# Kernel tuning notes

Hardware: AMD Instinct MI355X
Metric: run time of the kernel (lower is better)

Reference implementation:

```python
import jax, jax.numpy as jnp
import numpy as np

N_NODES = 50000
N_EDGES = 800000
IN_CH = 128
OUT_CH = 64
HID_CH = 2 * OUT_CH  # 128


def gcn_conv(x, edge_index, W, b, n_nodes):
    """PyG GCNConv: linear -> add self-loops -> sym-normalized scatter-add -> bias."""
    h = x @ W  # [N, out]
    loop = jnp.arange(n_nodes)
    row = jnp.concatenate([edge_index[0], loop])  # source nodes
    col = jnp.concatenate([edge_index[1], loop])  # target nodes
    deg = jax.ops.segment_sum(jnp.ones_like(col, dtype=h.dtype), col, num_segments=n_nodes)
    dinv = jnp.where(deg > 0, jax.lax.rsqrt(jnp.maximum(deg, 1.0)), 0.0)
    norm = dinv[row] * dinv[col]  # [E+N]
    msg = h[row] * norm[:, None]  # gather + scale, [E+N, out]
    out = jax.ops.segment_sum(msg, col, num_segments=n_nodes)  # scatter-add
    return out + b


def setup_inputs() -> dict:
    key = jax.random.key(0)
    ks = jax.random.split(key, 9)
    x = jax.random.normal(ks[0], (N_NODES, IN_CH), dtype=jnp.float32)
    edge_index = jax.random.randint(ks[1], (2, N_EDGES), 0, N_NODES, dtype=jnp.int64)
    s_in = 1.0 / np.sqrt(IN_CH)
    s_hid = 1.0 / np.sqrt(HID_CH)
    W1 = jax.random.normal(ks[2], (IN_CH, HID_CH), dtype=jnp.float32) * s_in
    b1 = jnp.zeros((HID_CH,), dtype=jnp.float32)
    W2 = jax.random.normal(ks[3], (HID_CH, OUT_CH), dtype=jnp.float32) * s_hid
    b2 = jnp.zeros((OUT_CH,), dtype=jnp.float32)
    W3 = jax.random.normal(ks[4], (HID_CH, OUT_CH), dtype=jnp.float32) * s_hid
    b3 = jnp.zeros((OUT_CH,), dtype=jnp.float32)
    return {"x": x, "edge_index": edge_index, "W1": W1, "b1": b1,
            "W2": W2, "b2": b2, "W3": W3, "b3": b3}


def reference(x, edge_index, W1, b1, W2, b2, W3, b3):
    act = jax.nn.relu
    hidden = act(gcn_conv(x, edge_index, W1, b1, N_NODES))
    x1 = act(gcn_conv(hidden, edge_index, W2, b2, N_NODES))
    x2 = act(gcn_conv(hidden, edge_index, W3, b3, N_NODES))
    return (x1, x2)
```

## Files before the change

kernel.cpp:

```cpp
#include <hip/hip_runtime.h>

#define N_NODES 50000
#define N_EDGES 800000
#define CH 128
#define SCAN_BLKS 98
#define WT_PAD 136
#define DUMMY N_NODES

typedef __attribute__((ext_vector_type(8))) short short8;
typedef __attribute__((ext_vector_type(4))) float floatx4;

__device__ __forceinline__ short f2bf(float f) {
    union { float f; unsigned u; } v; v.f = f;
    unsigned r = v.u + 0x7fff + ((v.u >> 16) & 1);
    return (short)(r >> 16);
}
__device__ __forceinline__ float bflo(unsigned u) {
    union { unsigned u; float f; } v; v.u = u << 16; return v.f;
}
__device__ __forceinline__ float bfhi(unsigned u) {
    union { unsigned u; float f; } v; v.u = u & 0xffff0000u; return v.f;
}


__global__ __launch_bounds__(256) void prep_kernel(const float* __restrict__ W1,
                                                   const float* __restrict__ W2,
                                                   const float* __restrict__ W3,
                                                   const float* __restrict__ b2,
                                                   const float* __restrict__ b3,
                                                   unsigned short* __restrict__ Wt1,
                                                   unsigned short* __restrict__ Wt23,
                                                   float* __restrict__ b23,
                                                   int* __restrict__ counts,
                                                   unsigned int* __restrict__ gdummy) {
    int i = blockIdx.x * blockDim.x + threadIdx.x;
    if (i < 128 * 128) {
        int n = i >> 7, k = i & 127;
        Wt1[i] = (unsigned short)f2bf(W1[k * 128 + n]);
        float w = (n < 64) ? W2[k * 64 + n] : W3[k * 64 + (n - 64)];
        Wt23[i] = (unsigned short)f2bf(w);
    } else if (i < 128 * 128 + 128) {
        int k2 = i - 128 * 128;
        b23[k2] = (k2 < 64) ? b2[k2] : b3[k2 - 64];
    } else if (i < 128 * 128 + 192) {
        gdummy[i - (128 * 128 + 128)] = 0;
    }
    for (int j = i; j < N_NODES; j += 66 * 256) counts[j] = 0;
}


__global__ void rank_kernel(const int* __restrict__ ei, int* __restrict__ counts,
                            int* __restrict__ rank) {
    int e = blockIdx.x * blockDim.x + threadIdx.x;
    if (e < N_EDGES) rank[e] = atomicAdd(&counts[ei[N_EDGES + e]], 1);
}

__global__ __launch_bounds__(256) void scan_block_kernel(const int* __restrict__ counts,
                                                         int* __restrict__ row_ptr,
                                                         float* __restrict__ dinv,
                                                         int* __restrict__ bsum) {
    __shared__ int s[256];
    int tid = threadIdx.x;
    int base = blockIdx.x * 512;
    int i0 = base + 2 * tid, i1 = i0 + 1;
    int v0 = (i0 < N_NODES) ? counts[i0] : 0;
    int v1 = (i1 < N_NODES) ? counts[i1] : 0;
    if (i0 < N_NODES) dinv[i0] = rsqrtf((float)(v0 + 1));
    if (i1 < N_NODES) dinv[i1] = rsqrtf((float)(v1 + 1));
    int p0 = (v0 + 3) & ~3, p1 = (v1 + 3) & ~3;
    int t = p0 + p1;
    s[tid] = t;
    __syncthreads();
    for (int off = 1; off < 256; off <<= 1) {
        int tmp = (tid >= off) ? s[tid - off] : 0;
        __syncthreads();
        s[tid] += tmp;
        __syncthreads();
    }
    int pre = s[tid] - t;
    if (i0 < N_NODES) row_ptr[i0] = pre;
    if (i1 < N_NODES) row_ptr[i1] = pre + p0;
    if (tid == 255) bsum[blockIdx.x] = s[255];
}

__global__ __launch_bounds__(256) void scan_fix_kernel(int* __restrict__ row_ptr,
                                                       const int* __restrict__ bsum,
                                                       const int* __restrict__ degs,
                                                       int* __restrict__ sorted_src) {
    __shared__ int s[128];
    int tid = threadIdx.x;
    if (tid < 128) s[tid] = (tid < SCAN_BLKS) ? bsum[tid] : 0;
    __syncthreads();
    for (int off = 1; off < 128; off <<= 1) {
        int t = (tid < 128 && tid >= off) ? s[tid - off] : 0;
        __syncthreads();
        if (tid < 128) s[tid] += t;
        __syncthreads();
    }
    int blockoff = (blockIdx.x == 0) ? 0 : s[blockIdx.x - 1];
    int base = blockIdx.x * 512;
    for (int i = base + tid; i < base + 512; i += 256) {
        if (i < N_NODES) {
            int v = row_ptr[i] + blockoff;
            row_ptr[i] = v;
            int d = degs[i];
            int pc = (d + 3) & ~3;
            for (int p = v + d; p < v + pc; ++p) sorted_src[p] = DUMMY;
        }
    }
}

__global__ void scatter_plain(const int* __restrict__ ei, const int* __restrict__ row_ptr,
                              const int* __restrict__ rank, int* __restrict__ sorted_src) {
    int e = blockIdx.x * blockDim.x + threadIdx.x;
    if (e < N_EDGES) {
        int dst = ei[N_EDGES + e];
        sorted_src[row_ptr[dst] + rank[e]] = ei[e];
    }
}


template <bool A_BF16>
__global__ __launch_bounds__(256) void gemm_mfma(const void* __restrict__ Ain,
                                                 const unsigned short* __restrict__ Wt,
                                                 const float* __restrict__ dinv,
                                                 unsigned short* __restrict__ g) {
    __shared__ unsigned short lds[128 * WT_PAD];
    int tid = threadIdx.x;
    int wave = tid >> 6, lane = tid & 63;
    int quad = lane >> 4, ln = lane & 15;

    {
        int r = tid >> 1, h = tid & 1;
        const int4* src = (const int4*)(Wt + r * 128 + h * 64);
#pragma unroll
        for (int i = 0; i < 8; ++i)
            *(int4*)&lds[r * WT_PAD + h * 64 + i * 8] = src[i];
    }

    int row_base = blockIdx.x * 64 + wave * 16;
    int arow = row_base + ln;
    bool ok = arow < N_NODES;
    short8 afrag[4];
    if (A_BF16) {
        const unsigned short* A = (const unsigned short*)Ain;
#pragma unroll
        for (int kk = 0; kk < 4; ++kk) {
            short8 v = {};
            if (ok) v = *(const short8*)(A + arow * 128 + kk * 32 + quad * 8);
            afrag[kk] = v;
        }
    } else {
        const float* A = (const float*)Ain;
#pragma unroll
        for (int kk = 0; kk < 4; ++kk) {
            short8 v = {};
            if (ok) {
                const float* p = A + arow * 128 + kk * 32 + quad * 8;
#pragma unroll
                for (int j = 0; j < 8; ++j) v[j] = f2bf(p[j]);
            }
            afrag[kk] = v;
        }
    }
    __syncthreads();

    floatx4 acc[8] = {};
#pragma unroll
    for (int n0 = 0; n0 < 8; ++n0) {
#pragma unroll
        for (int kk = 0; kk < 4; ++kk) {
            short8 b = *(const short8*)&lds[(n0 * 16 + ln) * WT_PAD + kk * 32 + quad * 8];
            acc[n0] = __builtin_amdgcn_mfma_f32_16x16x32_bf16(afrag[kk], b, acc[n0], 0, 0, 0);
        }
    }

    __syncthreads();
    unsigned short* st = &lds[wave * 16 * WT_PAD];
    float dv[4];
#pragma unroll
    for (int r = 0; r < 4; ++r) {
        int node = row_base + quad * 4 + r;
        dv[r] = (node < N_NODES) ? dinv[node] : 0.f;
    }
#pragma unroll
    for (int n0 = 0; n0 < 8; ++n0)
#pragma unroll
        for (int r = 0; r < 4; ++r)
            st[(quad * 4 + r) * WT_PAD + n0 * 16 + ln] =
                (unsigned short)f2bf(acc[n0][r] * dv[r]);
    __syncthreads();

#pragma unroll
    for (int i = 0; i < 4; ++i) {
        int row = i * 4 + quad;
        int node = row_base + row;
        short8 v = *(const short8*)&st[row * WT_PAD + ln * 8];
        if (node < N_NODES) *(short8*)(g + node * 128 + ln * 8) = v;
    }
}


template <int MODE>
__global__ __launch_bounds__(256) void aggregate_bf16(const unsigned short* __restrict__ g,
                                                      const float* __restrict__ dinv,
                                                      const int* __restrict__ row_ptr,
                                                      const int* __restrict__ degs,
                                                      const int* __restrict__ srcs,
                                                      const float* __restrict__ bias,
                                                      void* __restrict__ outp) {
    int sub = threadIdx.x >> 4;
    int n = blockIdx.x * 16 + sub;
    int c4 = threadIdx.x & 15;
    const uint4* grow = (const uint4*)g;
    uint4 u = grow[n * 16 + c4];
    float a0 = bflo(u.x), a1 = bfhi(u.x), a2 = bflo(u.y), a3 = bfhi(u.y);
    float a4 = bflo(u.z), a5 = bfhi(u.z), a6 = bflo(u.w), a7 = bfhi(u.w);
    float c0 = 0.f, c1 = 0.f, c2 = 0.f, c3 = 0.f, c5 = 0.f, c6 = 0.f, c7 = 0.f, c8 = 0.f;
    int beg = row_ptr[n];
    int pend = beg + ((degs[n] + 3) & ~3);
    int e = beg;
    for (; e + 8 <= pend; e += 8) {
        int4 sa = *(const int4*)&srcs[e];
        int4 sb = *(const int4*)&srcs[e + 4];
        uint4 v0 = grow[sa.x * 16 + c4];
        uint4 v1 = grow[sa.y * 16 + c4];
        uint4 v2 = grow[sa.z * 16 + c4];
        uint4 v3 = grow[sa.w * 16 + c4];
        uint4 v4 = grow[sb.x * 16 + c4];
        uint4 v5 = grow[sb.y * 16 + c4];
        uint4 v6 = grow[sb.z * 16 + c4];
        uint4 v7 = grow[sb.w * 16 + c4];
        a0 += bflo(v0.x); a1 += bfhi(v0.x); a2 += bflo(v0.y); a3 += bfhi(v0.y);
        a4 += bflo(v0.z); a5 += bfhi(v0.z); a6 += bflo(v0.w); a7 += bfhi(v0.w);
        c0 += bflo(v1.x); c1 += bfhi(v1.x); c2 += bflo(v1.y); c3 += bfhi(v1.y);
        c5 += bflo(v1.z); c6 += bfhi(v1.z); c7 += bflo(v1.w); c8 += bfhi(v1.w);
        a0 += bflo(v2.x); a1 += bfhi(v2.x); a2 += bflo(v2.y); a3 += bfhi(v2.y);
        a4 += bflo(v2.z); a5 += bfhi(v2.z); a6 += bflo(v2.w); a7 += bfhi(v2.w);
        c0 += bflo(v3.x); c1 += bfhi(v3.x); c2 += bflo(v3.y); c3 += bfhi(v3.y);
        c5 += bflo(v3.z); c6 += bfhi(v3.z); c7 += bflo(v3.w); c8 += bfhi(v3.w);
        a0 += bflo(v4.x); a1 += bfhi(v4.x); a2 += bflo(v4.y); a3 += bfhi(v4.y);
        a4 += bflo(v4.z); a5 += bfhi(v4.z); a6 += bflo(v4.w); a7 += bfhi(v4.w);
        c0 += bflo(v5.x); c1 += bfhi(v5.x); c2 += bflo(v5.y); c3 += bfhi(v5.y);
        c5 += bflo(v5.z); c6 += bfhi(v5.z); c7 += bflo(v5.w); c8 += bfhi(v5.w);
        a0 += bflo(v6.x); a1 += bfhi(v6.x); a2 += bflo(v6.y); a3 += bfhi(v6.y);
        a4 += bflo(v6.z); a5 += bfhi(v6.z); a6 += bflo(v6.w); a7 += bfhi(v6.w);
        c0 += bflo(v7.x); c1 += bfhi(v7.x); c2 += bflo(v7.y); c3 += bfhi(v7.y);
        c5 += bflo(v7.z); c6 += bfhi(v7.z); c7 += bflo(v7.w); c8 += bfhi(v7.w);
    }
    if (e < pend) {
        int4 sa = *(const int4*)&srcs[e];
        uint4 v0 = grow[sa.x * 16 + c4];
        uint4 v1 = grow[sa.y * 16 + c4];
        uint4 v2 = grow[sa.z * 16 + c4];
        uint4 v3 = grow[sa.w * 16 + c4];
        a0 += bflo(v0.x); a1 += bfhi(v0.x); a2 += bflo(v0.y); a3 += bfhi(v0.y);
        a4 += bflo(v0.z); a5 += bfhi(v0.z); a6 += bflo(v0.w); a7 += bfhi(v0.w);
        c0 += bflo(v1.x); c1 += bfhi(v1.x); c2 += bflo(v1.y); c3 += bfhi(v1.y);
        c5 += bflo(v1.z); c6 += bfhi(v1.z); c7 += bflo(v1.w); c8 += bfhi(v1.w);
        a0 += bflo(v2.x); a1 += bfhi(v2.x); a2 += bflo(v2.y); a3 += bfhi(v2.y);
        a4 += bflo(v2.z); a5 += bfhi(v2.z); a6 += bflo(v2.w); a7 += bfhi(v2.w);
        c0 += bflo(v3.x); c1 += bfhi(v3.x); c2 += bflo(v3.y); c3 += bfhi(v3.y);
        c5 += bflo(v3.z); c6 += bfhi(v3.z); c7 += bflo(v3.w); c8 += bfhi(v3.w);
    }
    a0 += c0; a1 += c1; a2 += c2; a3 += c3; a4 += c5; a5 += c6; a6 += c7; a7 += c8;
    float d = dinv[n];
    float4 bv0 = ((const float4*)bias)[c4 * 2];
    float4 bv1 = ((const float4*)bias)[c4 * 2 + 1];
    float o0 = fmaxf(d * a0 + bv0.x, 0.f);
    float o1 = fmaxf(d * a1 + bv0.y, 0.f);
    float o2 = fmaxf(d * a2 + bv0.z, 0.f);
    float o3 = fmaxf(d * a3 + bv0.w, 0.f);
    float o4 = fmaxf(d * a4 + bv1.x, 0.f);
    float o5 = fmaxf(d * a5 + bv1.y, 0.f);
    float o6 = fmaxf(d * a6 + bv1.z, 0.f);
    float o7 = fmaxf(d * a7 + bv1.w, 0.f);
    if (MODE == 0) {
        uint4 w;
        w.x = ((unsigned)(unsigned short)f2bf(o0)) | (((unsigned)(unsigned short)f2bf(o1)) << 16);
        w.y = ((unsigned)(unsigned short)f2bf(o2)) | (((unsigned)(unsigned short)f2bf(o3)) << 16);
        w.z = ((unsigned)(unsigned short)f2bf(o4)) | (((unsigned)(unsigned short)f2bf(o5)) << 16);
        w.w = ((unsigned)(unsigned short)f2bf(o6)) | (((unsigned)(unsigned short)f2bf(o7)) << 16);
        ((uint4*)outp)[n * 16 + c4] = w;
    } else {
        float* out = (float*)outp;
        float4 p0 = make_float4(o0, o1, o2, o3);
        float4 p1 = make_float4(o4, o5, o6, o7);
        if (c4 < 8) {
            ((float4*)out)[n * 16 + c4 * 2] = p0;
            ((float4*)out)[n * 16 + c4 * 2 + 1] = p1;
        } else {
            float* o2p = out + N_NODES * 64;
            ((float4*)o2p)[n * 16 + (c4 - 8) * 2] = p0;
            ((float4*)o2p)[n * 16 + (c4 - 8) * 2 + 1] = p1;
        }
    }
}


extern "C" void kernel_launch(void* const* d_in, const int* in_sizes, int n_in,
                              void* d_out, int out_size, void* d_ws, size_t ws_size,
                              hipStream_t stream) {
    const float* x  = (const float*)d_in[0];
    const int*   ei = (const int*)d_in[1];
    const float* W1 = (const float*)d_in[2];
    const float* b1 = (const float*)d_in[3];
    const float* W2 = (const float*)d_in[4];
    const float* b2 = (const float*)d_in[5];
    const float* W3 = (const float*)d_in[6];
    const float* b3 = (const float*)d_in[7];
    float* out = (float*)d_out;

    char* w = (char*)d_ws;
    int*            counts     = (int*)(w + 0);
    int*            row_ptr    = (int*)(w + 204800);
    float*          dinv       = (float*)(w + 409600);
    int*            rank       = (int*)(w + 614400);
    int*            sorted_src = (int*)(w + 3814400);
    unsigned short* Wt1        = (unsigned short*)(w + 7614400);
    unsigned short* Wt23       = (unsigned short*)(w + 7647168);
    float*          b23        = (float*)(w + 7679936);
    int*            bsum       = (int*)(w + 7680448);
    unsigned short* g1         = (unsigned short*)(w + 8388608);
    unsigned short* hidden     = (unsigned short*)(w + 22020096);

    prep_kernel<<<66, 256, 0, stream>>>(W1, W2, W3, b2, b3, Wt1, Wt23, b23, counts,
                                        (unsigned int*)(g1 + N_NODES * 128));
    rank_kernel<<<(N_EDGES + 255) / 256, 256, 0, stream>>>(ei, counts, rank);
    scan_block_kernel<<<SCAN_BLKS, 256, 0, stream>>>(counts, row_ptr, dinv, bsum);
    scan_fix_kernel<<<SCAN_BLKS, 256, 0, stream>>>(row_ptr, bsum, counts, sorted_src);
    scatter_plain<<<(N_EDGES + 255) / 256, 256, 0, stream>>>(ei, row_ptr, rank, sorted_src);

    const int gemm_blocks = (N_NODES + 63) / 64;
    const int agg_blocks = N_NODES / 16;

    gemm_mfma<false><<<gemm_blocks, 256, 0, stream>>>(x, Wt1, dinv, g1);
    aggregate_bf16<0><<<agg_blocks, 256, 0, stream>>>(g1, dinv, row_ptr, counts, sorted_src, b1, hidden);

    gemm_mfma<true><<<gemm_blocks, 256, 0, stream>>>(hidden, Wt23, dinv, g1);
    aggregate_bf16<1><<<agg_blocks, 256, 0, stream>>>(g1, dinv, row_ptr, counts, sorted_src, b23, out);
}
```

Before: 226.1 us.

## Split aggregation into channel halves and store CSR sources as 16-bit indices

The aggregation kernel now runs in two grid halves, each covering 64 of the 128 channels, with 8 threads per node and 32 nodes per block. Each node's 256-byte gathered rows are split into two 128-byte pieces, so the working set per half is smaller and should sit better in L2. Source indices in the sorted CSR array are narrowed to unsigned short, since node ids up to 50000 fit, which halves the index traffic. In exchange, the row_ptr, degree and index reads are repeated for both halves, and the code now relies on the node count staying below 65536.

Measured after the change: 217.3 us. -3.9%, faster.

```diff
diff --git a/kernel.cpp b/kernel.cpp
--- a/kernel.cpp
+++ b/kernel.cpp
@@ -6,6 +6,7 @@
 #define SCAN_BLKS 98
 #define WT_PAD 136
 #define DUMMY N_NODES
+#define AGG_HALF_BLKS 1563
 
 typedef __attribute__((ext_vector_type(8))) short short8;
 typedef __attribute__((ext_vector_type(4))) float floatx4;
@@ -86,7 +87,7 @@
 __global__ __launch_bounds__(256) void scan_fix_kernel(int* __restrict__ row_ptr,
                                                        const int* __restrict__ bsum,
                                                        const int* __restrict__ degs,
-                                                       int* __restrict__ sorted_src) {
+                                                       unsigned short* __restrict__ sorted_src) {
     __shared__ int s[128];
     int tid = threadIdx.x;
     if (tid < 128) s[tid] = (tid < SCAN_BLKS) ? bsum[tid] : 0;
@@ -105,17 +106,18 @@
             row_ptr[i] = v;
             int d = degs[i];
             int pc = (d + 3) & ~3;
-            for (int p = v + d; p < v + pc; ++p) sorted_src[p] = DUMMY;
+            for (int p = v + d; p < v + pc; ++p) sorted_src[p] = (unsigned short)DUMMY;
         }
     }
 }
 
 __global__ void scatter_plain(const int* __restrict__ ei, const int* __restrict__ row_ptr,
-                              const int* __restrict__ rank, int* __restrict__ sorted_src) {
+                              const int* __restrict__ rank,
+                              unsigned short* __restrict__ sorted_src) {
     int e = blockIdx.x * blockDim.x + threadIdx.x;
     if (e < N_EDGES) {
         int dst = ei[N_EDGES + e];
-        sorted_src[row_ptr[dst] + rank[e]] = ei[e];
+        sorted_src[row_ptr[dst] + rank[e]] = (unsigned short)ei[e];
     }
 }
 
@@ -206,14 +208,17 @@
                                                       const float* __restrict__ dinv,
                                                       const int* __restrict__ row_ptr,
                                                       const int* __restrict__ degs,
-                                                      const int* __restrict__ srcs,
+                                                      const unsigned short* __restrict__ srcs,
                                                       const float* __restrict__ bias,
                                                       void* __restrict__ outp) {
-    int sub = threadIdx.x >> 4;
-    int n = blockIdx.x * 16 + sub;
-    int c4 = threadIdx.x & 15;
+    int h = 0, nb = blockIdx.x;
+    if (nb >= AGG_HALF_BLKS) { h = 1; nb -= AGG_HALF_BLKS; }
+    int n = nb * 32 + (threadIdx.x >> 3);
+    if (n >= N_NODES) return;
+    int c4 = threadIdx.x & 7;
+    int hoff = h * 8;
     const uint4* grow = (const uint4*)g;
-    uint4 u = grow[n * 16 + c4];
+    uint4 u = grow[n * 16 + hoff + c4];
     float a0 = bflo(u.x), a1 = bfhi(u.x), a2 = bflo(u.y), a3 = bfhi(u.y);
     float a4 = bflo(u.z), a5 = bfhi(u.z), a6 = bflo(u.w), a7 = bfhi(u.w);
     float c0 = 0.f, c1 = 0.f, c2 = 0.f, c3 = 0.f, c5 = 0.f, c6 = 0.f, c7 = 0.f, c8 = 0.f;
@@ -221,16 +226,16 @@
     int pend = beg + ((degs[n] + 3) & ~3);
     int e = beg;
     for (; e + 8 <= pend; e += 8) {
-        int4 sa = *(const int4*)&srcs[e];
-        int4 sb = *(const int4*)&srcs[e + 4];
-        uint4 v0 = grow[sa.x * 16 + c4];
-        uint4 v1 = grow[sa.y * 16 + c4];
-        uint4 v2 = grow[sa.z * 16 + c4];
-        uint4 v3 = grow[sa.w * 16 + c4];
-        uint4 v4 = grow[sb.x * 16 + c4];
-        uint4 v5 = grow[sb.y * 16 + c4];
-        uint4 v6 = grow[sb.z * 16 + c4];
-        uint4 v7 = grow[sb.w * 16 + c4];
+        ushort4 sa = *(const ushort4*)&srcs[e];
+        ushort4 sb = *(const ushort4*)&srcs[e + 4];
+        uint4 v0 = grow[sa.x * 16 + hoff + c4];
+        uint4 v1 = grow[sa.y * 16 + hoff + c4];
+        uint4 v2 = grow[sa.z * 16 + hoff + c4];
+        uint4 v3 = grow[sa.w * 16 + hoff + c4];
+        uint4 v4 = grow[sb.x * 16 + hoff + c4];
+        uint4 v5 = grow[sb.y * 16 + hoff + c4];
+        uint4 v6 = grow[sb.z * 16 + hoff + c4];
+        uint4 v7 = grow[sb.w * 16 + hoff + c4];
         a0 += bflo(v0.x); a1 += bfhi(v0.x); a2 += bflo(v0.y); a3 += bfhi(v0.y);
         a4 += bflo(v0.z); a5 += bfhi(v0.z); a6 += bflo(v0.w); a7 += bfhi(v0.w);
         c0 += bflo(v1.x); c1 += bfhi(v1.x); c2 += bflo(v1.y); c3 += bfhi(v1.y);
@@ -249,11 +254,11 @@
         c5 += bflo(v7.z); c6 += bfhi(v7.z); c7 += bflo(v7.w); c8 += bfhi(v7.w);
     }
     if (e < pend) {
-        int4 sa = *(const int4*)&srcs[e];
-        uint4 v0 = grow[sa.x * 16 + c4];
-        uint4 v1 = grow[sa.y * 16 + c4];
-        uint4 v2 = grow[sa.z * 16 + c4];
-        uint4 v3 = grow[sa.w * 16 + c4];
+        ushort4 sa = *(const ushort4*)&srcs[e];
+        uint4 v0 = grow[sa.x * 16 + hoff + c4];
+        uint4 v1 = grow[sa.y * 16 + hoff + c4];
+        uint4 v2 = grow[sa.z * 16 + hoff + c4];
+        uint4 v3 = grow[sa.w * 16 + hoff + c4];
         a0 += bflo(v0.x); a1 += bfhi(v0.x); a2 += bflo(v0.y); a3 += bfhi(v0.y);
         a4 += bflo(v0.z); a5 += bfhi(v0.z); a6 += bflo(v0.w); a7 += bfhi(v0.w);
         c0 += bflo(v1.x); c1 += bfhi(v1.x); c2 += bflo(v1.y); c3 += bfhi(v1.y);
@@ -265,8 +270,8 @@
     }
     a0 += c0; a1 += c1; a2 += c2; a3 += c3; a4 += c5; a5 += c6; a6 += c7; a7 += c8;
     float d = dinv[n];
-    float4 bv0 = ((const float4*)bias)[c4 * 2];
-    float4 bv1 = ((const float4*)bias)[c4 * 2 + 1];
+    float4 bv0 = ((const float4*)bias)[h * 16 + c4 * 2];
+    float4 bv1 = ((const float4*)bias)[h * 16 + c4 * 2 + 1];
     float o0 = fmaxf(d * a0 + bv0.x, 0.f);
     float o1 = fmaxf(d * a1 + bv0.y, 0.f);
     float o2 = fmaxf(d * a2 + bv0.z, 0.f);
@@ -281,19 +286,11 @@
         w.y = ((unsigned)(unsigned short)f2bf(o2)) | (((unsigned)(unsigned short)f2bf(o3)) << 16);
         w.z = ((unsigned)(unsigned short)f2bf(o4)) | (((unsigned)(unsigned short)f2bf(o5)) << 16);
         w.w = ((unsigned)(unsigned short)f2bf(o6)) | (((unsigned)(unsigned short)f2bf(o7)) << 16);
-        ((uint4*)outp)[n * 16 + c4] = w;
+        ((uint4*)outp)[n * 16 + hoff + c4] = w;
     } else {
-        float* out = (float*)outp;
-        float4 p0 = make_float4(o0, o1, o2, o3);
-        float4 p1 = make_float4(o4, o5, o6, o7);
-        if (c4 < 8) {
-            ((float4*)out)[n * 16 + c4 * 2] = p0;
-            ((float4*)out)[n * 16 + c4 * 2 + 1] = p1;
-        } else {
-            float* o2p = out + N_NODES * 64;
-            ((float4*)o2p)[n * 16 + (c4 - 8) * 2] = p0;
-            ((float4*)o2p)[n * 16 + (c4 - 8) * 2 + 1] = p1;
-        }
+        float* out = (float*)outp + (size_t)h * N_NODES * 64;
+        ((float4*)out)[n * 16 + c4 * 2] = make_float4(o0, o1, o2, o3);
+        ((float4*)out)[n * 16 + c4 * 2 + 1] = make_float4(o4, o5, o6, o7);
     }
 }
 
@@ -316,7 +313,7 @@
     int*            row_ptr    = (int*)(w + 204800);
     float*          dinv       = (float*)(w + 409600);
     int*            rank       = (int*)(w + 614400);
-    int*            sorted_src = (int*)(w + 3814400);
+    unsigned short* sorted_src = (unsigned short*)(w + 3814400);
     unsigned short* Wt1        = (unsigned short*)(w + 7614400);
     unsigned short* Wt23       = (unsigned short*)(w + 7647168);
     float*          b23        = (float*)(w + 7679936);
@@ -332,7 +329,7 @@
     scatter_plain<<<(N_EDGES + 255) / 256, 256, 0, stream>>>(ei, row_ptr, rank, sorted_src);
 
     const int gemm_blocks = (N_NODES + 63) / 64;
-    const int agg_blocks = N_NODES / 16;
+    const int agg_blocks = 2 * AGG_HALF_BLKS;
 
     gemm_mfma<false><<<gemm_blocks, 256, 0, stream>>>(x, Wt1, dinv, g1);
     aggregate_bf16<0><<<agg_blocks, 256, 0, stream>>>(g1, dinv, row_ptr, counts, sorted_src, b1, hidden);
```
